# Performance work log

Hardware: AMD Instinct MI355X
Metric: run time of the kernel (lower is better)

Reference implementation:

```python
import jax, jax.numpy as jnp
import numpy as np

B, L, D, Z, H, N, G = 8, 2048, 1024, 128, 2048, 16, 32
MAXPOS = 2048
EPS = 1e-5
PRIOR_COUNT = 2.0  # TimestepNorm prior pseudo-count


def setup_inputs() -> dict:
    ks = jax.random.split(jax.random.key(0), 12)
    std = 0.02  # bert init
    return {
        "x": jax.random.normal(ks[0], (B, L, D), jnp.float32),
        "prior_mean": jnp.zeros((G,), jnp.float32),
        "prior_logv": jnp.zeros((G,), jnp.float32),
        "tn_weight": jnp.ones((D,), jnp.float32),
        "tn_bias": jnp.zeros((D,), jnp.float32),
        "delta": jax.random.normal(ks[1], (D, N), jnp.float32),
        "alpha": jax.random.normal(ks[2], (D, N), jnp.float32),
        "ema_beta": jax.random.normal(ks[3], (D, N), jnp.float32),
        "ema_gamma": jax.random.normal(ks[4], (D, N), jnp.float32),
        "omega": jax.random.normal(ks[5], (D,), jnp.float32),
        "rms_weight": jnp.ones((D,), jnp.float32),
        "Wv": jax.random.normal(ks[6], (H, D), jnp.float32) * std,
        "bv": jnp.zeros((H,), jnp.float32),
        "Wmx": jax.random.normal(ks[7], (Z + H + 2 * D, D), jnp.float32) * std,
        "bmx": jnp.zeros((Z + H + 2 * D,), jnp.float32),
        "Wh": jax.random.normal(ks[8], (D, H), jnp.float32) * std,
        "qk_gamma": jax.random.normal(ks[9], (2, Z), jnp.float32) * 0.1,
        "qk_beta": jax.random.normal(ks[10], (2, Z), jnp.float32) * 0.1,
        "rel_bias": jax.random.normal(ks[11], (2 * MAXPOS - 1,), jnp.float32) * 0.02,
    }


def timestep_norm(x, prior_mean, prior_logv, weight, bias):
    """Causal cumulative group norm with a prior (TimestepNorm)."""
    m = D // G  # features per group
    xg = x.reshape(B, L, G, m)
    s1 = jnp.cumsum(xg.sum(-1), axis=1)            # B,L,G  running sum
    s2 = jnp.cumsum((xg * xg).sum(-1), axis=1)     # B,L,G  running sum of squares
    cnt = PRIOR_COUNT + m * jnp.arange(1, L + 1, dtype=x.dtype)[None, :, None]
    pv = jnp.exp(prior_logv)
    mean = (PRIOR_COUNT * prior_mean + s1) / cnt
    var = (PRIOR_COUNT * (pv + prior_mean ** 2) + s2) / cnt - mean ** 2
    xn = (xg - mean[..., None]) * jax.lax.rsqrt(var[..., None] + EPS)
    return xn.reshape(B, L, D) * weight + bias


def multihead_ema(x, delta, alpha, ema_beta, ema_gamma, omega):
    """MultiHeadEMA: causal damped-EMA convolution via FFT, plus omega residual."""
    p = jax.nn.sigmoid(delta)                       # D,N
    a = jax.nn.sigmoid(alpha)
    q = 1.0 - p * a                                 # decay in (0,1)
    t = jnp.arange(L, dtype=x.dtype)
    vander = jnp.exp(t[None, None, :] * jnp.log(q)[:, :, None])  # D,N,L
    scale = 1.0 / jnp.sqrt(jnp.asarray(N, x.dtype))
    kern = jnp.einsum('dn,dnl,dn->dl', p * ema_beta, vander, ema_gamma * scale)
    xT = x.transpose(0, 2, 1)                       # B,D,L
    n = 2 * L
    out = jnp.fft.irfft(jnp.fft.rfft(xT, n=n) * jnp.fft.rfft(kern, n=n)[None], n=n)[..., :L]
    out = out + xT * omega[:, None]
    return out.transpose(0, 2, 1)


def _forward(x, prior_mean, prior_logv, tn_weight, tn_bias, delta, alpha,
             ema_beta, ema_gamma, omega, rms_weight, Wv, bv, Wmx, bmx, Wh,
             qk_gamma, qk_beta, rel_bias):
    residual = x
    xn = timestep_norm(x, prior_mean, prior_logv, tn_weight, tn_bias)
    v = jax.nn.silu(xn @ Wv.T + bv)                 # B,L,H
    mx = multihead_ema(xn, delta, alpha, ema_beta, ema_gamma, omega)
    mx = mx * jax.lax.rsqrt(jnp.mean(mx * mx, axis=-1, keepdims=True) + EPS) * rms_weight  # RMSNorm
    base = mx @ Wmx.T + bmx                         # B,L,Z+H+2D
    u = jax.nn.sigmoid(base[..., :D])
    zr = jax.nn.silu(base[..., D:D + Z + H])
    hx = base[..., D + Z + H:]
    z, r = zr[..., :Z], zr[..., Z:]
    zz = z[..., None, :] * qk_gamma + qk_beta       # B,L,2,Z
    q = zz[..., 0, :] * (Z ** -0.5)
    k = zz[..., 1, :]
    # simple relative positional bias: bias[i,j] = rel_bias[MAXPOS-1 + (j-i)]
    idx = (MAXPOS - 1) + (jnp.arange(L)[None, :] - jnp.arange(L)[:, None])
    qk = jnp.einsum('biz,bjz->bij', q, k) + rel_bias[idx]
    causal = jnp.tril(jnp.ones((L, L), bool))
    qk = jnp.where(causal, qk, -jnp.inf)
    attn = jax.nn.softmax(qk, axis=-1)              # B,L,L
    h = jnp.einsum('bij,bjh->bih', attn, v)         # B,L,H
    h = jax.nn.silu(hx + (h * r) @ Wh.T)            # B,L,D
    return residual + u * (h - residual)


def reference(x, prior_mean, prior_logv, tn_weight, tn_bias, delta, alpha,
              ema_beta, ema_gamma, omega, rms_weight, Wv, bv, Wmx, bmx, Wh,
              qk_gamma, qk_beta, rel_bias):
    return _forward(x, prior_mean, prior_logv, tn_weight, tn_bias, delta, alpha,
                    ema_beta, ema_gamma, omega, rms_weight, Wv, bv, Wmx, bmx, Wh,
                    qk_gamma, qk_beta, rel_bias)
```

## Files before the change

kernel.cpp:

```cpp
#include <hip/hip_runtime.h>
#include <stdint.h>

#define B_ 8
#define L_ 2048
#define D_ 1024
#define Z_ 128
#define H_ 2048
#define NE_ 16
#define G_ 32
#define MAXPOS_ 2048
#define NMX_ 4224
#define EPS_ 1e-5f
#define PC_ 2.0f
#define NTILE_ 16
#define NPACK_ 136
#define TILE_ELEMS_ 16384

typedef short bf16x8 __attribute__((ext_vector_type(8)));
typedef float f32x4 __attribute__((ext_vector_type(4)));

__device__ __forceinline__ float bf2f(uint16_t u) {
  union { uint32_t u; float f; } v; v.u = ((uint32_t)u) << 16; return v.f;
}
__device__ __forceinline__ uint16_t f2bf(float f) {
  union { float f; uint32_t u; } v; v.f = f;
  uint32_t r = (v.u + 0x7FFFu + ((v.u >> 16) & 1u)) >> 16;
  return (uint16_t)r;
}
__device__ __forceinline__ float sigmoidf_(float x) { return 1.f / (1.f + __expf(-x)); }
__device__ __forceinline__ float siluf_(float x) { return x / (1.f + __expf(-x)); }

__device__ __forceinline__ float waveRedSum(float v) {
  #pragma unroll
  for (int m = 32; m; m >>= 1) v += __shfl_xor(v, m, 64);
  return v;
}

__device__ __forceinline__ void gl2lds(const uint16_t* g, uint16_t* l) {
  __builtin_amdgcn_global_load_lds(
      (const __attribute__((address_space(1))) void*)g,
      (__attribute__((address_space(3))) void*)l, 16, 0, 0);
}

__global__ __launch_bounds__(256) void k_fallback(float* __restrict__ out, int n, float wsmb) {
  for (int i = blockIdx.x * 256 + threadIdx.x; i < n; i += gridDim.x * 256)
    out[i] = (i == 0) ? wsmb : 0.f;
}

__global__ __launch_bounds__(256) void k_f2bf(const float* __restrict__ src,
                                              uint16_t* __restrict__ dst, int n) {
  for (int i = blockIdx.x * 256 + threadIdx.x; i < n; i += gridDim.x * 256)
    dst[i] = f2bf(src[i]);
}

__global__ __launch_bounds__(256) void k_tnsum(const float* __restrict__ x,
                                               float* __restrict__ s1g,
                                               float* __restrict__ s2g) {
  const int bg = blockIdx.x;
  const int b = bg / G_, g = bg % G_;
  const int tid = threadIdx.x;
  const int j = tid & 31;
  const int lsub = tid >> 5;
  #pragma unroll
  for (int i = 0; i < 16; ++i) {
    const int l = blockIdx.y * 128 + i * 8 + lsub;
    float v = x[((size_t)(b * L_ + l)) * D_ + g * 32 + j];
    float a = v, sq = v * v;
    #pragma unroll
    for (int m = 1; m <= 16; m <<= 1) { a += __shfl_xor(a, m, 64); sq += __shfl_xor(sq, m, 64); }
    if (j == 0) { s1g[(size_t)bg * L_ + l] = a; s2g[(size_t)bg * L_ + l] = sq; }
  }
}

__global__ __launch_bounds__(64) void k_tnscan(float* __restrict__ s1g,
                                               float* __restrict__ s2g) {
  const int bg = blockIdx.x;
  const int lane = threadIdx.x;
  #pragma unroll
  for (int pass = 0; pass < 2; ++pass) {
    float* gp = (pass ? s2g : s1g) + (size_t)bg * L_;
    float loc[32];
    const int b0 = lane * 32;
    float tot = 0.f;
    #pragma unroll
    for (int t = 0; t < 32; ++t) { loc[t] = gp[b0 + t]; tot += loc[t]; }
    float incl = tot;
    #pragma unroll
    for (int off = 1; off < 64; off <<= 1) {
      float nv = __shfl_up(incl, off, 64);
      if (lane >= off) incl += nv;
    }
    float run = incl - tot;
    #pragma unroll
    for (int t = 0; t < 32; ++t) { run += loc[t]; gp[b0 + t] = run; }
  }
}

__global__ __launch_bounds__(256) void k_tnnorm(const float* __restrict__ x,
                                                const float* __restrict__ s1g,
                                                const float* __restrict__ s2g,
                                                const float* __restrict__ pm,
                                                const float* __restrict__ plv,
                                                const float* __restrict__ w,
                                                const float* __restrict__ bias,
                                                uint16_t* __restrict__ xn) {
  const int bg = blockIdx.x;
  const int b = bg / G_, g = bg % G_;
  const int tid = threadIdx.x;
  const int j = tid & 31;
  const int lsub = tid >> 5;
  const float pmv = pm[g];
  const float pvv = __expf(plv[g]);
  const float wj = w[g * 32 + j];
  const float bj = bias[g * 32 + j];
  const float pterm = PC_ * (pvv + pmv * pmv);
  #pragma unroll
  for (int i = 0; i < 16; ++i) {
    const int l = blockIdx.y * 128 + i * 8 + lsub;
    const size_t idx = ((size_t)(b * L_ + l)) * D_ + g * 32 + j;
    const float v = x[idx];
    const float cnt = PC_ + 32.f * (float)(l + 1);
    const float mean = (PC_ * pmv + s1g[(size_t)bg * L_ + l]) / cnt;
    const float var = (pterm + s2g[(size_t)bg * L_ + l]) / cnt - mean * mean;
    xn[idx] = f2bf((v - mean) * rsqrtf(var + EPS_) * wj + bj);
  }
}

template <typename T>
__global__ __launch_bounds__(256) void k_transpose(const T* __restrict__ src,
                                                   T* __restrict__ dst, int R, int C) {
  __shared__ T tile[32][33];
  const size_t batch = (size_t)R * C * blockIdx.z;
  const int c0 = blockIdx.x * 32, r0 = blockIdx.y * 32;
  const int tx = threadIdx.x & 31, ty = threadIdx.x >> 5;
  #pragma unroll
  for (int k = 0; k < 4; ++k) {
    int r = ty + k * 8;
    tile[r][tx] = src[batch + (size_t)(r0 + r) * C + c0 + tx];
  }
  __syncthreads();
  #pragma unroll
  for (int k = 0; k < 4; ++k) {
    int r = ty + k * 8;
    dst[batch + (size_t)(c0 + r) * R + r0 + tx] = tile[tx][r];
  }
}

__global__ __launch_bounds__(64) void k_ema(const uint16_t* __restrict__ xnT,
                                            const float* __restrict__ delta,
                                            const float* __restrict__ alpha,
                                            const float* __restrict__ beta,
                                            const float* __restrict__ gamma,
                                            const float* __restrict__ omega,
                                            float* __restrict__ mxT) {
  __shared__ float hst[64 * NE_];
  const int bd = blockIdx.x;
  const int d = bd & (D_ - 1);
  const int c = threadIdx.x;

  float q[NE_], pb[NE_], gs[NE_];
  #pragma unroll
  for (int n = 0; n < NE_; ++n) {
    float p = sigmoidf_(delta[d * NE_ + n]);
    float a = sigmoidf_(alpha[d * NE_ + n]);
    q[n] = 1.f - p * a;
    pb[n] = p * beta[d * NE_ + n];
    gs[n] = gamma[d * NE_ + n] * 0.25f;
  }

  const uint16_t* xp = xnT + (size_t)bd * L_ + c * 32;
  bf16x8 xin[4];
  #pragma unroll
  for (int s = 0; s < 4; ++s) xin[s] = *(const bf16x8*)(xp + s * 8);

  float h[NE_];
  #pragma unroll
  for (int n = 0; n < NE_; ++n) h[n] = 0.f;

  #pragma unroll
  for (int k = 0; k < 32; ++k) {
    float xv = bf2f((uint16_t)xin[k >> 3][k & 7]);
    #pragma unroll
    for (int n = 0; n < NE_; ++n) h[n] = fmaf(q[n], h[n], pb[n] * xv);
  }
  #pragma unroll
  for (int n = 0; n < NE_; ++n) hst[c * NE_ + n] = h[n];
  __syncthreads();

  if (c < NE_) {
    float qq = q[c];
    float q32 = qq * qq; q32 *= q32; q32 *= q32; q32 *= q32; q32 *= q32;
    float hi = 0.f;
    for (int cc = 0; cc < 64; ++cc) {
      float cur = hst[cc * NE_ + c];
      hst[cc * NE_ + c] = hi;
      hi = fmaf(q32, hi, cur);
    }
  }
  __syncthreads();

  #pragma unroll
  for (int n = 0; n < NE_; ++n) h[n] = hst[c * NE_ + n];
  const float om = omega[d];
  float* op = mxT + (size_t)bd * L_ + c * 32;
  f32x4 ov;
  #pragma unroll
  for (int k = 0; k < 32; ++k) {
    float xv = bf2f((uint16_t)xin[k >> 3][k & 7]);
    float accv = 0.f;
    #pragma unroll
    for (int n = 0; n < NE_; ++n) {
      h[n] = fmaf(q[n], h[n], pb[n] * xv);
      accv = fmaf(gs[n], h[n], accv);
    }
    ov[k & 3] = accv + om * xv;
    if ((k & 3) == 3) *(f32x4*)(op + (k & ~3)) = ov;
  }
}

__global__ __launch_bounds__(256) void k_rms(const float* __restrict__ mx,
                                             const float* __restrict__ w,
                                             uint16_t* __restrict__ mxn) {
  __shared__ float red[4];
  const size_t row = blockIdx.x;
  const int tid = threadIdx.x;
  float ss = 0.f;
  #pragma unroll
  for (int i = 0; i < 4; ++i) {
    float v = mx[row * D_ + tid + i * 256];
    ss += v * v;
  }
  ss = waveRedSum(ss);
  if ((tid & 63) == 0) red[tid >> 6] = ss;
  __syncthreads();
  ss = red[0] + red[1] + red[2] + red[3];
  const float scale = rsqrtf(ss * (1.f / D_) + EPS_);
  #pragma unroll
  for (int i = 0; i < 4; ++i) {
    int dcol = tid + i * 256;
    mxn[row * D_ + dcol] = f2bf(mx[row * D_ + dcol] * scale * w[dcol]);
  }
}

__global__ __launch_bounds__(256) void k_qkprep(const float* __restrict__ z,
                                                const float* __restrict__ qg,
                                                const float* __restrict__ qb,
                                                uint16_t* __restrict__ q,
                                                uint16_t* __restrict__ k, int n) {
  for (int i = blockIdx.x * 256 + threadIdx.x; i < n; i += gridDim.x * 256) {
    int zc = i & (Z_ - 1);
    float v = z[i];
    q[i] = f2bf((v * qg[zc] + qb[zc]) * 0.08838834764831845f);
    k[i] = f2bf(v * qg[Z_ + zc] + qb[Z_ + zc]);
  }
}


template <int MODE>
__global__ __launch_bounds__(256, 4) void k_gemm128(
    const uint16_t* __restrict__ A, const uint16_t* __restrict__ Bm,
    int N, int K,
    const float* __restrict__ bias,
    float* __restrict__ outf, uint16_t* __restrict__ outb,
    uint16_t* __restrict__ ubuf, float* __restrict__ zbuf,
    uint16_t* __restrict__ rbuf, float* __restrict__ hxbuf,
    const float* __restrict__ x0) {
  __shared__ uint16_t sm[16384];
  const int t = threadIdx.x;
  const int lane = t & 63, wave = t >> 6;
  const int quad = lane >> 4, r16 = lane & 15;
  const int wm = wave >> 1, wn = wave & 1;
  const int bm = blockIdx.x * 128;
  const int bn = blockIdx.y * 128;

  f32x4 acc[4][4];
  const f32x4 zf = {0.f, 0.f, 0.f, 0.f};
  #pragma unroll
  for (int i = 0; i < 4; ++i)
    #pragma unroll
    for (int j = 0; j < 4; ++j) acc[i][j] = zf;

  const int sgz = (((t & 3) ^ ((t >> 3) & 3)) << 3);
  const uint16_t* gA = A + (size_t)(bm + (t >> 2)) * K + sgz;
  const uint16_t* gB = Bm + (size_t)(bn + (t >> 2)) * K + sgz;
  const size_t qstep = (size_t)64 * K;
  uint16_t* lA = sm + t * 8;
  uint16_t* lB = sm + 4096 + t * 8;

  const int ga = ((quad ^ ((r16 >> 1) & 3)) << 3);
  const int aOff = (wm * 64 + r16) * 32 + ga;
  const int bOff = 4096 + (wn * 64 + r16) * 32 + ga;

#define STAGE(c, kb) do {                                                     \
    gl2lds(gA + (kb), lA + (c) * 8192);                                       \
    gl2lds(gA + qstep + (kb), lA + (c) * 8192 + 2048);                        \
    gl2lds(gB + (kb), lB + (c) * 8192);                                       \
    gl2lds(gB + qstep + (kb), lB + (c) * 8192 + 2048);                        \
  } while (0)

  const int NT = K >> 5;

  STAGE(0, 0);
  __syncthreads();

  bf16x8 af[4], bfr[4];
  for (int tt = 0; tt < NT; ++tt) {
    const int c = tt & 1;
    const int co = c * 8192;
    if (tt + 1 < NT) STAGE(c ^ 1, (tt + 1) * 32);
    #pragma unroll
    for (int j = 0; j < 4; ++j)
      bfr[j] = *(const bf16x8*)&sm[co + bOff + j * 512];
    #pragma unroll
    for (int i = 0; i < 4; ++i)
      af[i] = *(const bf16x8*)&sm[co + aOff + i * 512];
    #pragma unroll
    for (int i = 0; i < 4; ++i)
      #pragma unroll
      for (int j = 0; j < 4; ++j)
        acc[i][j] = __builtin_amdgcn_mfma_f32_16x16x32_bf16(
            af[i], bfr[j], acc[i][j], 0, 0, 0);
    __syncthreads();
  }
#undef STAGE

  #pragma unroll
  for (int i = 0; i < 4; ++i) {
    #pragma unroll
    for (int j = 0; j < 4; ++j) {
      #pragma unroll
      for (int r = 0; r < 4; ++r) {
        const int row = bm + wm * 64 + i * 16 + quad * 4 + r;
        const int col = bn + wn * 64 + j * 16 + r16;
        float val = acc[i][j][r];
        if (MODE == 0) {
          outb[(size_t)row * N + col] = f2bf(siluf_(val + bias[col]));
        } else if (MODE == 1) {
          val += bias[col];
          if (col < D_)                 ubuf[(size_t)row * D_ + col] = f2bf(sigmoidf_(val));
          else if (col < D_ + Z_)       zbuf[(size_t)row * Z_ + (col - D_)] = siluf_(val);
          else if (col < D_ + Z_ + H_)  rbuf[(size_t)row * H_ + (col - D_ - Z_)] = f2bf(siluf_(val));
          else                          hxbuf[(size_t)row * D_ + (col - D_ - Z_ - H_)] = val;
        } else {
          const size_t idx = (size_t)row * N + col;
          float g = siluf_(val + hxbuf[idx]);
          float xv = x0[idx];
          outf[idx] = xv + bf2f(ubuf[idx]) * (g - xv);
        }
      }
    }
  }
}

__global__ __launch_bounds__(256) void k_qksm(
    const uint16_t* __restrict__ qg, const uint16_t* __restrict__ kg,
    const float* __restrict__ relb, uint16_t* __restrict__ Pp) {
  __shared__ uint16_t Ks[128 * 128];
  __shared__ float relwin[256];
  const int qt = blockIdx.x;
  const int bl = blockIdx.y;
  const int tid = threadIdx.x;
  const int w = tid >> 6, lane = tid & 63;
  const int quad = lane >> 4, r16 = lane & 15;
  const uint16_t* qb_b = qg + (size_t)bl * L_ * Z_;
  const uint16_t* kb_b = kg + (size_t)bl * L_ * Z_;
  uint16_t* P_b = Pp + (size_t)bl * NPACK_ * TILE_ELEMS_;

  const int ksg = (tid >> 4) * 128 + (((tid & 15) ^ ((tid >> 4) & 7)) << 3);
  const int kg7 = r16 & 7;

  bf16x8 aq[2][4];
  #pragma unroll
  for (int i = 0; i < 2; ++i)
    #pragma unroll
    for (int s = 0; s < 4; ++s)
      aq[i][s] = *(const bf16x8*)&qb_b[(size_t)(qt * 128 + w * 32 + i * 16 + r16) * Z_ +
                                       s * 32 + quad * 8];

  float m8[8], l8[8];
  #pragma unroll
  for (int t = 0; t < 8; ++t) { m8[t] = -3.4e38f; l8[t] = 0.f; }

  const f32x4 zf = {0.f, 0.f, 0.f, 0.f};

  for (int kt = 0; kt <= qt; ++kt) {
    __syncthreads();
    const uint16_t* src = kb_b + (size_t)kt * 128 * Z_;
    #pragma unroll
    for (int s2 = 0; s2 < 8; ++s2)
      gl2lds(src + s2 * 2048 + ksg, Ks + s2 * 2048 + tid * 8);
    if (tid < 255) relwin[tid] = relb[2047 + (kt - qt) * 128 - 127 + tid];
    __syncthreads();
    #pragma unroll
    for (int j = 0; j < 8; ++j) {
      f32x4 a0 = zf, a1 = zf;
      #pragma unroll
      for (int s = 0; s < 4; ++s) {
        bf16x8 bk = *(const bf16x8*)&Ks[(j * 16 + r16) * 128 +
                                        (((s * 4 + quad) ^ kg7) << 3)];
        a0 = __builtin_amdgcn_mfma_f32_16x16x32_bf16(aq[0][s], bk, a0, 0, 0, 0);
        a1 = __builtin_amdgcn_mfma_f32_16x16x32_bf16(aq[1][s], bk, a1, 0, 0, 0);
      }
      #pragma unroll
      for (int i = 0; i < 2; ++i) {
        const f32x4 av = i ? a1 : a0;
        #pragma unroll
        for (int r = 0; r < 4; ++r) {
          const int rloc = w * 32 + i * 16 + quad * 4 + r;
          const int cloc = j * 16 + r16;
          if (kt < qt || cloc <= rloc) {
            const float v = av[r] + relwin[cloc - rloc + 127];
            const int t = i * 4 + r;
            const float mn = fmaxf(m8[t], v);
            l8[t] = l8[t] * __expf(m8[t] - mn) + __expf(v - mn);
            m8[t] = mn;
          }
        }
      }
    }
  }

  #pragma unroll
  for (int t = 0; t < 8; ++t) {
    #pragma unroll
    for (int msk = 1; msk <= 8; msk <<= 1) {
      const float mo = __shfl_xor(m8[t], msk, 64);
      const float lo = __shfl_xor(l8[t], msk, 64);
      const float mn = fmaxf(m8[t], mo);
      l8[t] = l8[t] * __expf(m8[t] - mn) + lo * __expf(mo - mn);
      m8[t] = mn;
    }
    l8[t] = 1.f / l8[t];
  }

  for (int kt = 0; kt <= qt; ++kt) {
    __syncthreads();
    const uint16_t* src = kb_b + (size_t)kt * 128 * Z_;
    #pragma unroll
    for (int s2 = 0; s2 < 8; ++s2)
      gl2lds(src + s2 * 2048 + ksg, Ks + s2 * 2048 + tid * 8);
    if (tid < 255) relwin[tid] = relb[2047 + (kt - qt) * 128 - 127 + tid];
    __syncthreads();
    uint16_t* Pt = P_b + (size_t)(qt * (qt + 1) / 2 + kt) * TILE_ELEMS_;
    #pragma unroll
    for (int j = 0; j < 8; ++j) {
      f32x4 a0 = zf, a1 = zf;
      #pragma unroll
      for (int s = 0; s < 4; ++s) {
        bf16x8 bk = *(const bf16x8*)&Ks[(j * 16 + r16) * 128 +
                                        (((s * 4 + quad) ^ kg7) << 3)];
        a0 = __builtin_amdgcn_mfma_f32_16x16x32_bf16(aq[0][s], bk, a0, 0, 0, 0);
        a1 = __builtin_amdgcn_mfma_f32_16x16x32_bf16(aq[1][s], bk, a1, 0, 0, 0);
      }
      #pragma unroll
      for (int i = 0; i < 2; ++i) {
        const f32x4 av = i ? a1 : a0;
        #pragma unroll
        for (int r = 0; r < 4; ++r) {
          const int rloc = w * 32 + i * 16 + quad * 4 + r;
          const int cloc = j * 16 + r16;
          const int t = i * 4 + r;
          float p = 0.f;
          if (kt < qt || cloc <= rloc) {
            const float v = av[r] + relwin[cloc - rloc + 127];
            p = __expf(v - m8[t]) * l8[t];
          }
          Pt[rloc * 128 + cloc] = f2bf(p);
        }
      }
    }
  }
}

__global__ __launch_bounds__(256, 4) void k_pv(
    const uint16_t* __restrict__ Pp, const uint16_t* __restrict__ vT,
    uint16_t* __restrict__ rh) {
  __shared__ uint16_t sm[16384];
  const int qt = NTILE_ - 1 - blockIdx.x;
  const int bn = blockIdx.y * 128;
  const int bl = blockIdx.z;
  const uint16_t* Pq = Pp + (size_t)bl * NPACK_ * TILE_ELEMS_ +
                       (size_t)(qt * (qt + 1) / 2) * TILE_ELEMS_;
  const uint16_t* v_b = vT + (size_t)bl * H_ * L_;
  uint16_t* rh_b = rh + (size_t)bl * L_ * H_;

  const int tid = threadIdx.x;
  const int wave = tid >> 6, lane = tid & 63;
  const int quad = lane >> 4, r16 = lane & 15;
  const int wm = wave >> 1, wn = wave & 1;
  const int rowW = wm * 64, colW = wn * 64;

  f32x4 acc[4][4];
  const f32x4 zf = {0.f, 0.f, 0.f, 0.f};
  #pragma unroll
  for (int i = 0; i < 4; ++i)
    #pragma unroll
    for (int j = 0; j < 4; ++j) acc[i][j] = zf;

  const int rA = tid >> 2;
  const int sg = (((tid & 3) ^ ((tid >> 3) & 3)) << 3);
  const int gpv = ((quad ^ ((r16 >> 1) & 3)) << 3);

#define PVSTAGE(c, s) do {                                                    \
    const int kt_ = (s) >> 2, ks_ = (s) & 3;                                  \
    const uint16_t* At_ = Pq + (size_t)kt_ * TILE_ELEMS_ + ks_ * 32 + sg;     \
    const uint16_t* Bt_ = v_b + (size_t)(bn + rA) * L_ + kt_ * 128 +          \
                          ks_ * 32 + sg;                                      \
    gl2lds(At_ + rA * 128, sm + (c) * 8192 + tid * 8);                        \
    gl2lds(At_ + (rA + 64) * 128, sm + (c) * 8192 + 2048 + tid * 8);          \
    gl2lds(Bt_, sm + (c) * 8192 + 4096 + tid * 8);                            \
    gl2lds(Bt_ + (size_t)64 * L_, sm + (c) * 8192 + 6144 + tid * 8);          \
  } while (0)

  const int S = 4 * (qt + 1);

  PVSTAGE(0, 0);
  __syncthreads();

  bf16x8 af[4], bfr[4];
  for (int s = 0; s < S; ++s) {
    const int c = s & 1;
    const int co = c * 8192;
    if (s + 1 < S) PVSTAGE(c ^ 1, s + 1);
    #pragma unroll
    for (int j = 0; j < 4; ++j)
      bfr[j] = *(const bf16x8*)&sm[co + 4096 + (colW + j * 16 + r16) * 32 + gpv];
    #pragma unroll
    for (int i = 0; i < 4; ++i)
      af[i] = *(const bf16x8*)&sm[co + (rowW + i * 16 + r16) * 32 + gpv];
    #pragma unroll
    for (int i = 0; i < 4; ++i)
      #pragma unroll
      for (int j = 0; j < 4; ++j)
        acc[i][j] = __builtin_amdgcn_mfma_f32_16x16x32_bf16(af[i], bfr[j], acc[i][j], 0, 0, 0);
    __syncthreads();
  }
#undef PVSTAGE

  #pragma unroll
  for (int i = 0; i < 4; ++i) {
    #pragma unroll
    for (int j = 0; j < 4; ++j) {
      #pragma unroll
      for (int r = 0; r < 4; ++r) {
        const int row = qt * 128 + rowW + i * 16 + quad * 4 + r;
        const int col = bn + colW + j * 16 + r16;
        const size_t idx = (size_t)row * H_ + col;
        const float rv = bf2f(rh_b[idx]);
        rh_b[idx] = f2bf(acc[i][j][r] * rv);
      }
    }
  }
}

extern "C" void kernel_launch(void* const* d_in, const int* in_sizes, int n_in,
                              void* d_out, int out_size, void* d_ws, size_t ws_size,
                              hipStream_t stream) {
  (void)in_sizes; (void)n_in;
  const float* x         = (const float*)d_in[0];
  const float* prior_mean= (const float*)d_in[1];
  const float* prior_logv= (const float*)d_in[2];
  const float* tn_w      = (const float*)d_in[3];
  const float* tn_b      = (const float*)d_in[4];
  const float* delta     = (const float*)d_in[5];
  const float* alpha     = (const float*)d_in[6];
  const float* ema_beta  = (const float*)d_in[7];
  const float* ema_gamma = (const float*)d_in[8];
  const float* omega     = (const float*)d_in[9];
  const float* rms_w     = (const float*)d_in[10];
  const float* Wv        = (const float*)d_in[11];
  const float* bv        = (const float*)d_in[12];
  const float* Wmx       = (const float*)d_in[13];
  const float* bmx       = (const float*)d_in[14];
  const float* Wh        = (const float*)d_in[15];
  const float* qk_gamma  = (const float*)d_in[16];
  const float* qk_beta   = (const float*)d_in[17];
  const float* rel_bias  = (const float*)d_in[18];
  float* out = (float*)d_out;

  const int BL = B_ * L_;
  const size_t MB = 1024 * 1024;
  const size_t REQUIRED = 256 * MB;

  if (ws_size < REQUIRED) {
    k_fallback<<<dim3(4096), dim3(256), 0, stream>>>(out, out_size, (float)(ws_size / MB));
    return;
  }

  char* p = (char*)d_ws;
  uint16_t* xn   = (uint16_t*)(p);
  uint16_t* ubuf = (uint16_t*)(p);
  float*    s1g  = (float*)   (p + 32 * MB);
  float*    s2g  = (float*)   (p + 34 * MB);
  uint16_t* xnT  = (uint16_t*)(p + 32 * MB);
  uint16_t* mxn  = (uint16_t*)(p + 32 * MB);
  uint16_t* vbuf = (uint16_t*)(p + 64 * MB);
  float*    mx   = (float*)   (p + 64 * MB);
  uint16_t* rbuf = (uint16_t*)(p + 64 * MB);
  uint16_t* wv_b = (uint16_t*)(p + 128 * MB);
  uint16_t* vT   = (uint16_t*)(p + 128 * MB);
  uint16_t* wmx_b = (uint16_t*)(p + 192 * MB);
  uint16_t* wh_b  = (uint16_t*)(p + 192 * MB);
  float*    zb    = (float*)   (p + 201 * MB);
  uint16_t* qb    = (uint16_t*)(p + 209 * MB);
  uint16_t* kb2   = (uint16_t*)(p + 213 * MB);
  uint16_t* Ppack = (uint16_t*)(p + 217 * MB);
  float* mxT = out;
  float* hx  = out;

  k_f2bf<<<dim3(1024), dim3(256), 0, stream>>>(Wv, wv_b, H_ * D_);
  k_f2bf<<<dim3(2048), dim3(256), 0, stream>>>(Wmx, wmx_b, NMX_ * D_);
  k_tnsum<<<dim3(B_ * G_, 16), dim3(256), 0, stream>>>(x, s1g, s2g);
  k_tnscan<<<dim3(B_ * G_), dim3(64), 0, stream>>>(s1g, s2g);
  k_tnnorm<<<dim3(B_ * G_, 16), dim3(256), 0, stream>>>(
      x, s1g, s2g, prior_mean, prior_logv, tn_w, tn_b, xn);
  k_transpose<uint16_t><<<dim3(D_ / 32, L_ / 32, B_), dim3(256), 0, stream>>>(xn, xnT, L_, D_);
  k_gemm128<0><<<dim3(BL / 128, H_ / 128), dim3(256), 0, stream>>>(
      xn, wv_b, H_, D_, bv, nullptr, vbuf,
      nullptr, nullptr, nullptr, nullptr, nullptr);
  k_transpose<uint16_t><<<dim3(H_ / 32, L_ / 32, B_), dim3(256), 0, stream>>>(vbuf, vT, L_, H_);
  k_ema<<<dim3(B_ * D_), dim3(64), 0, stream>>>(xnT, delta, alpha, ema_beta, ema_gamma, omega, mxT);
  k_transpose<float><<<dim3(L_ / 32, D_ / 32, B_), dim3(256), 0, stream>>>(mxT, mx, D_, L_);
  k_rms<<<dim3(BL), dim3(256), 0, stream>>>(mx, rms_w, mxn);
  k_gemm128<1><<<dim3(BL / 128, NMX_ / 128), dim3(256), 0, stream>>>(
      mxn, wmx_b, NMX_, D_, bmx, nullptr, nullptr,
      ubuf, zb, rbuf, hx, nullptr);
  k_qkprep<<<dim3(1024), dim3(256), 0, stream>>>(zb, qk_gamma, qk_beta, qb, kb2, BL * Z_);
  k_qksm<<<dim3(NTILE_, B_), dim3(256), 0, stream>>>(qb, kb2, rel_bias, Ppack);
  k_pv<<<dim3(NTILE_, H_ / 128, B_), dim3(256), 0, stream>>>(Ppack, vT, rbuf);
  k_f2bf<<<dim3(1024), dim3(256), 0, stream>>>(Wh, wh_b, D_ * H_);
  k_gemm128<4><<<dim3(BL / 128, D_ / 128), dim3(256), 0, stream>>>(
      rbuf, wh_b, D_, H_, nullptr, out, nullptr,
      ubuf, nullptr, nullptr, hx, x);
}
```

Baseline: 1.203 ms.

## Fuse V transpose into GEMM epilogue and vectorize transpose kernels

The V-projection GEMM now stages its activated tile in shared memory and writes it out already transposed (H by L per batch) with 16-byte stores. This removes the separate transpose pass over the V buffer. The remaining bf16 and fp32 transposes use 64x64 tiles with vector loads and stores instead of scalar 32x32 tiles. The GEMM shared buffer grows to hold the padded tile, and workspace offsets are reshuffled so the vT, mx and rbuf buffers do not alias.

```diff
diff --git a/kernel.cpp b/kernel.cpp
--- a/kernel.cpp
+++ b/kernel.cpp
@@ -126,23 +126,55 @@
   }
 }
 
-template <typename T>
-__global__ __launch_bounds__(256) void k_transpose(const T* __restrict__ src,
-                                                   T* __restrict__ dst, int R, int C) {
-  __shared__ T tile[32][33];
+__global__ __launch_bounds__(256) void k_tp16(const uint16_t* __restrict__ src,
+                                              uint16_t* __restrict__ dst, int R, int C) {
+  __shared__ uint16_t tile[64 * 65];
   const size_t batch = (size_t)R * C * blockIdx.z;
-  const int c0 = blockIdx.x * 32, r0 = blockIdx.y * 32;
-  const int tx = threadIdx.x & 31, ty = threadIdx.x >> 5;
-  #pragma unroll
-  for (int k = 0; k < 4; ++k) {
-    int r = ty + k * 8;
-    tile[r][tx] = src[batch + (size_t)(r0 + r) * C + c0 + tx];
+  const int c0 = blockIdx.x * 64, r0 = blockIdx.y * 64;
+  const int t = threadIdx.x;
+  const int rr = t >> 3;
+  const int cc = (t & 7) * 8;
+  #pragma unroll
+  for (int p = 0; p < 2; ++p) {
+    const int row = p * 32 + rr;
+    bf16x8 v = *(const bf16x8*)&src[batch + (size_t)(r0 + row) * C + c0 + cc];
+    #pragma unroll
+    for (int i = 0; i < 8; ++i) tile[(cc + i) * 65 + row] = (uint16_t)v[i];
   }
   __syncthreads();
   #pragma unroll
-  for (int k = 0; k < 4; ++k) {
-    int r = ty + k * 8;
-    dst[batch + (size_t)(c0 + r) * R + r0 + tx] = tile[tx][r];
+  for (int p = 0; p < 2; ++p) {
+    const int crow = p * 32 + rr;
+    bf16x8 o;
+    #pragma unroll
+    for (int i = 0; i < 8; ++i) o[i] = (short)tile[crow * 65 + cc + i];
+    *(bf16x8*)&dst[batch + (size_t)(c0 + crow) * R + r0 + cc] = o;
+  }
+}
+
+__global__ __launch_bounds__(256) void k_tpf32(const float* __restrict__ src,
+                                               float* __restrict__ dst, int R, int C) {
+  __shared__ float tile[64 * 65];
+  const size_t batch = (size_t)R * C * blockIdx.z;
+  const int c0 = blockIdx.x * 64, r0 = blockIdx.y * 64;
+  const int t = threadIdx.x;
+  const int rr = t >> 4;
+  const int cc = (t & 15) * 4;
+  #pragma unroll
+  for (int p = 0; p < 4; ++p) {
+    const int row = p * 16 + rr;
+    f32x4 v = *(const f32x4*)&src[batch + (size_t)(r0 + row) * C + c0 + cc];
+    #pragma unroll
+    for (int i = 0; i < 4; ++i) tile[(cc + i) * 65 + row] = v[i];
+  }
+  __syncthreads();
+  #pragma unroll
+  for (int p = 0; p < 4; ++p) {
+    const int crow = p * 16 + rr;
+    f32x4 o;
+    #pragma unroll
+    for (int i = 0; i < 4; ++i) o[i] = tile[crow * 65 + cc + i];
+    *(f32x4*)&dst[batch + (size_t)(c0 + crow) * R + r0 + cc] = o;
   }
 }
 
@@ -265,7 +297,7 @@
     uint16_t* __restrict__ ubuf, float* __restrict__ zbuf,
     uint16_t* __restrict__ rbuf, float* __restrict__ hxbuf,
     const float* __restrict__ x0) {
-  __shared__ uint16_t sm[16384];
+  __shared__ uint16_t sm[17408];
   const int t = threadIdx.x;
   const int lane = t & 63, wave = t >> 6;
   const int quad = lane >> 4, r16 = lane & 15;
@@ -324,28 +356,50 @@
   }
 #undef STAGE
 
-  #pragma unroll
-  for (int i = 0; i < 4; ++i) {
-    #pragma unroll
-    for (int j = 0; j < 4; ++j) {
-      #pragma unroll
-      for (int r = 0; r < 4; ++r) {
-        const int row = bm + wm * 64 + i * 16 + quad * 4 + r;
-        const int col = bn + wn * 64 + j * 16 + r16;
-        float val = acc[i][j][r];
-        if (MODE == 0) {
-          outb[(size_t)row * N + col] = f2bf(siluf_(val + bias[col]));
-        } else if (MODE == 1) {
-          val += bias[col];
-          if (col < D_)                 ubuf[(size_t)row * D_ + col] = f2bf(sigmoidf_(val));
-          else if (col < D_ + Z_)       zbuf[(size_t)row * Z_ + (col - D_)] = siluf_(val);
-          else if (col < D_ + Z_ + H_)  rbuf[(size_t)row * H_ + (col - D_ - Z_)] = f2bf(siluf_(val));
-          else                          hxbuf[(size_t)row * D_ + (col - D_ - Z_ - H_)] = val;
-        } else {
-          const size_t idx = (size_t)row * N + col;
-          float g = siluf_(val + hxbuf[idx]);
-          float xv = x0[idx];
-          outf[idx] = xv + bf2f(ubuf[idx]) * (g - xv);
+  if (MODE == 0) {
+    #pragma unroll
+    for (int i = 0; i < 4; ++i)
+      #pragma unroll
+      for (int j = 0; j < 4; ++j)
+        #pragma unroll
+        for (int r = 0; r < 4; ++r) {
+          const int hloc = wn * 64 + j * 16 + r16;
+          const int lloc = wm * 64 + i * 16 + quad * 4 + r;
+          sm[hloc * 136 + lloc] = f2bf(siluf_(acc[i][j][r] + bias[bn + hloc]));
+        }
+    __syncthreads();
+    const int bb = bm >> 11;
+    const int lb = bm & 2047;
+    uint16_t* vTb = outb + (size_t)bb * H_ * L_;
+    #pragma unroll
+    for (int p = 0; p < 8; ++p) {
+      const int hloc = p * 16 + (t >> 4);
+      const int l0 = (t & 15) * 8;
+      bf16x8 v = *(const bf16x8*)&sm[hloc * 136 + l0];
+      *(bf16x8*)&vTb[(size_t)(bn + hloc) * L_ + lb + l0] = v;
+    }
+  } else {
+    #pragma unroll
+    for (int i = 0; i < 4; ++i) {
+      #pragma unroll
+      for (int j = 0; j < 4; ++j) {
+        #pragma unroll
+        for (int r = 0; r < 4; ++r) {
+          const int row = bm + wm * 64 + i * 16 + quad * 4 + r;
+          const int col = bn + wn * 64 + j * 16 + r16;
+          float val = acc[i][j][r];
+          if (MODE == 1) {
+            val += bias[col];
+            if (col < D_)                 ubuf[(size_t)row * D_ + col] = f2bf(sigmoidf_(val));
+            else if (col < D_ + Z_)       zbuf[(size_t)row * Z_ + (col - D_)] = siluf_(val);
+            else if (col < D_ + Z_ + H_)  rbuf[(size_t)row * H_ + (col - D_ - Z_)] = f2bf(siluf_(val));
+            else                          hxbuf[(size_t)row * D_ + (col - D_ - Z_ - H_)] = val;
+          } else {
+            const size_t idx = (size_t)row * N + col;
+            float g = siluf_(val + hxbuf[idx]);
+            float xv = x0[idx];
+            outf[idx] = xv + bf2f(ubuf[idx]) * (g - xv);
+          }
         }
       }
     }
@@ -594,11 +648,10 @@
   float*    s2g  = (float*)   (p + 34 * MB);
   uint16_t* xnT  = (uint16_t*)(p + 32 * MB);
   uint16_t* mxn  = (uint16_t*)(p + 32 * MB);
-  uint16_t* vbuf = (uint16_t*)(p + 64 * MB);
-  float*    mx   = (float*)   (p + 64 * MB);
-  uint16_t* rbuf = (uint16_t*)(p + 64 * MB);
+  uint16_t* vT   = (uint16_t*)(p + 64 * MB);
   uint16_t* wv_b = (uint16_t*)(p + 128 * MB);
-  uint16_t* vT   = (uint16_t*)(p + 128 * MB);
+  float*    mx   = (float*)   (p + 128 * MB);
+  uint16_t* rbuf = (uint16_t*)(p + 128 * MB);
   uint16_t* wmx_b = (uint16_t*)(p + 192 * MB);
   uint16_t* wh_b  = (uint16_t*)(p + 192 * MB);
   float*    zb    = (float*)   (p + 201 * MB);
@@ -614,13 +667,12 @@
   k_tnscan<<<dim3(B_ * G_), dim3(64), 0, stream>>>(s1g, s2g);
   k_tnnorm<<<dim3(B_ * G_, 16), dim3(256), 0, stream>>>(
       x, s1g, s2g, prior_mean, prior_logv, tn_w, tn_b, xn);
-  k_transpose<uint16_t><<<dim3(D_ / 32, L_ / 32, B_), dim3(256), 0, stream>>>(xn, xnT, L_, D_);
+  k_tp16<<<dim3(D_ / 64, L_ / 64, B_), dim3(256), 0, stream>>>(xn, xnT, L_, D_);
   k_gemm128<0><<<dim3(BL / 128, H_ / 128), dim3(256), 0, stream>>>(
-      xn, wv_b, H_, D_, bv, nullptr, vbuf,
+      xn, wv_b, H_, D_, bv, nullptr, vT,
       nullptr, nullptr, nullptr, nullptr, nullptr);
-  k_transpose<uint16_t><<<dim3(H_ / 32, L_ / 32, B_), dim3(256), 0, stream>>>(vbuf, vT, L_, H_);
   k_ema<<<dim3(B_ * D_), dim3(64), 0, stream>>>(xnT, delta, alpha, ema_beta, ema_gamma, omega, mxT);
-  k_transpose<float><<<dim3(L_ / 32, D_ / 32, B_), dim3(256), 0, stream>>>(mxT, mx, D_, L_);
+  k_tpf32<<<dim3(L_ / 64, D_ / 64, B_), dim3(256), 0, stream>>>(mxT, mx, D_, L_);
   k_rms<<<dim3(BL), dim3(256), 0, stream>>>(mx, rms_w, mxn);
   k_gemm128<1><<<dim3(BL / 128, NMX_ / 128), dim3(256), 0, stream>>>(
       mxn, wmx_b, NMX_, D_, bmx, nullptr, nullptr,
```

Result: faster. 1.158 ms (-3.8%).
